# Kernel optimization log

Hardware: AMD Instinct MI355X
Metric: run time of the kernel (lower is better)

## Reference

```python
import jax, jax.numpy as jnp
import numpy as np

BITS = 8
BOUND = 2 ** (BITS - 1) - 1  # 127, symmetric int8 as in AQT IntNumerics


def setup_inputs() -> dict:
    key = jax.random.key(0)
    k1, k2 = jax.random.split(key)
    lhs = jax.random.normal(k1, (8192, 4096), dtype=jnp.float32)
    rhs = jax.random.normal(k2, (4096, 4096), dtype=jnp.float32)
    return {"lhs": lhs, "rhs": rhs}


def reference(lhs, rhs):
    # Per-channel symmetric scales over the contracting dim (AQT calibration:
    # abs-max / bound). lhs contracts axis 1, rhs contracts axis 0, per
    # dimension_numbers (((1,),(0,)),((),())).
    lhs_scale = jnp.max(jnp.abs(lhs), axis=1, keepdims=True) / BOUND  # [M,1]
    rhs_scale = jnp.max(jnp.abs(rhs), axis=0, keepdims=True) / BOUND  # [1,N]
    lhs_scale = jnp.where(lhs_scale == 0, jnp.ones_like(lhs_scale), lhs_scale)
    rhs_scale = jnp.where(rhs_scale == 0, jnp.ones_like(rhs_scale), rhs_scale)

    # Quantize: round-to-nearest, clip to [-127, 127], store as int8.
    qlhs = jnp.clip(jnp.round(lhs / lhs_scale), -BOUND, BOUND).astype(jnp.int8)
    qrhs = jnp.clip(jnp.round(rhs / rhs_scale), -BOUND, BOUND).astype(jnp.int8)

    # Integer matmul with int32 accumulation (the AQT quantized dot_general).
    acc = jax.lax.dot_general(
        qlhs, qrhs,
        dimension_numbers=(((1,), (0,)), ((), ())),
        preferred_element_type=jnp.int32,
    )  # [M, N] int32

    # Inline dequant by transposed scales (scale_t): [M,1] * [1,N].
    return acc.astype(jnp.float32) * lhs_scale * rhs_scale
```

## Files before the change

kernel.cpp:

```cpp
#include <hip/hip_runtime.h>
#include <stdint.h>

#define M_DIM 8192
#define N_DIM 4096
#define K_DIM 4096

typedef int v4i __attribute__((ext_vector_type(4)));

typedef __attribute__((address_space(1))) const void gas_void;
typedef __attribute__((address_space(3))) void las_void;

__device__ __forceinline__ void async_copy16(const uint8_t* g, uint8_t* l) {
    __builtin_amdgcn_global_load_lds((gas_void*)g, (las_void*)l, 16, 0, 0);
}

__device__ __forceinline__ int quant1(float x, float scale) {
    float q = __builtin_rintf(x / scale);
    q = fminf(127.0f, fmaxf(-127.0f, q));
    return (int)q;
}

__device__ __forceinline__ uint32_t pack4(int q0, int q1, int q2, int q3) {
    return (uint32_t)(q0 & 255) | ((uint32_t)(q1 & 255) << 8) |
           ((uint32_t)(q2 & 255) << 16) | ((uint32_t)(q3 & 255) << 24);
}

__global__ __launch_bounds__(256) void quant_lhs_kernel(
    const float* __restrict__ lhs, uint8_t* __restrict__ qlhs,
    float* __restrict__ lhs_scale) {
    const int row = blockIdx.x;
    const int tid = threadIdx.x;
    const float4* src = (const float4*)(lhs + (size_t)row * K_DIM);

    float4 v[4];
    float m = 0.0f;
#pragma unroll
    for (int i = 0; i < 4; ++i) {
        v[i] = src[tid + i * 256];
        m = fmaxf(m, fmaxf(fmaxf(fabsf(v[i].x), fabsf(v[i].y)),
                           fmaxf(fabsf(v[i].z), fabsf(v[i].w))));
    }
#pragma unroll
    for (int off = 32; off > 0; off >>= 1)
        m = fmaxf(m, __shfl_down(m, off, 64));

    __shared__ float wmax[4];
    if ((tid & 63) == 0) wmax[tid >> 6] = m;
    __syncthreads();
    const float mm = fmaxf(fmaxf(wmax[0], wmax[1]), fmaxf(wmax[2], wmax[3]));
    const float scale = (mm == 0.0f) ? 1.0f : mm / 127.0f;
    if (tid == 0) lhs_scale[row] = scale;

    uint32_t* dst = (uint32_t*)(qlhs + (size_t)row * K_DIM);
#pragma unroll
    for (int i = 0; i < 4; ++i) {
        dst[tid + i * 256] = pack4(quant1(v[i].x, scale), quant1(v[i].y, scale),
                                   quant1(v[i].z, scale), quant1(v[i].w, scale));
    }
}

__global__ __launch_bounds__(256) void rhs_max_kernel(
    const float* __restrict__ rhs, uint32_t* __restrict__ maxbits) {
    const int c4 = (blockIdx.x * 256 + threadIdx.x) * 4;
    const int r0 = blockIdx.y * 32;
    float m0 = 0.0f, m1 = 0.0f, m2 = 0.0f, m3 = 0.0f;
#pragma unroll
    for (int r = 0; r < 32; ++r) {
        const float4 v = *(const float4*)(rhs + (size_t)(r0 + r) * N_DIM + c4);
        m0 = fmaxf(m0, fabsf(v.x));
        m1 = fmaxf(m1, fabsf(v.y));
        m2 = fmaxf(m2, fabsf(v.z));
        m3 = fmaxf(m3, fabsf(v.w));
    }
    atomicMax(&maxbits[c4 + 0], __float_as_uint(m0));
    atomicMax(&maxbits[c4 + 1], __float_as_uint(m1));
    atomicMax(&maxbits[c4 + 2], __float_as_uint(m2));
    atomicMax(&maxbits[c4 + 3], __float_as_uint(m3));
}

__global__ __launch_bounds__(256) void quant_rhs_t_kernel(
    const float* __restrict__ rhs, const uint32_t* __restrict__ maxbits,
    uint8_t* __restrict__ qrhsT) {
    __shared__ __align__(16) uint8_t tile[64 * 132];
    const int nbase = blockIdx.x * 64;
    const int kbase = blockIdx.y * 128;
    const int tid = threadIdx.x;

    const int n0 = (tid & 15) * 4;
    float s[4];
#pragma unroll
    for (int j = 0; j < 4; ++j) {
        const float m = __uint_as_float(maxbits[nbase + n0 + j]);
        s[j] = (m == 0.0f) ? 1.0f : m / 127.0f;
    }

#pragma unroll
    for (int p = 0; p < 2; ++p) {
        const int k0 = (tid >> 4) * 4 + p * 64;
        int q[4][4];
#pragma unroll
        for (int i = 0; i < 4; ++i) {
            const float4 v = *(const float4*)(
                rhs + (size_t)(kbase + k0 + i) * N_DIM + nbase + n0);
            q[i][0] = quant1(v.x, s[0]);
            q[i][1] = quant1(v.y, s[1]);
            q[i][2] = quant1(v.z, s[2]);
            q[i][3] = quant1(v.w, s[3]);
        }
#pragma unroll
        for (int j = 0; j < 4; ++j) {
            *(uint32_t*)(tile + (n0 + j) * 132 + k0) =
                pack4(q[0][j], q[1][j], q[2][j], q[3][j]);
        }
    }
    __syncthreads();

#pragma unroll
    for (int p = 0; p < 2; ++p) {
        const int c = tid + p * 256;
        const int n = c >> 3;
        const int g = c & 7;
        uint32_t d[4];
#pragma unroll
        for (int w = 0; w < 4; ++w)
            d[w] = *(const uint32_t*)(tile + n * 132 + g * 16 + w * 4);
        uint4 u;
        u.x = d[0]; u.y = d[1]; u.z = d[2]; u.w = d[3];
        *(uint4*)(qrhsT + (size_t)(nbase + n) * K_DIM + kbase + g * 16) = u;
    }
}

__global__ __launch_bounds__(512, 2) void gemm_i8_kernel(
    const uint8_t* __restrict__ qlhs, const uint8_t* __restrict__ qrhsT,
    const float* __restrict__ lhs_scale, const uint32_t* __restrict__ maxbits,
    float* __restrict__ out) {
    extern __shared__ __align__(16) uint8_t smem[];

    const int tid = threadIdx.x;
    const int wave = tid >> 6;
    const int lane = tid & 63;

    const int obid = blockIdx.y * 16 + blockIdx.x;
    const int xcd = obid & 7;
    const int local = obid >> 3;
    const int ty = (xcd >> 1) * 8 + (local >> 3);
    const int tx = (xcd & 1) * 8 + (local & 7);
    const int bm = ty * 256;
    const int bn = tx * 256;

    const int srow = tid >> 2;
    const int gsrc = (((tid & 3) ^ ((tid >> 3) & 3)) << 4);
    const uint8_t* gA = qlhs + (size_t)(bm + srow) * K_DIM + gsrc;
    const uint8_t* gA2 = gA + (size_t)128 * K_DIM;
    const uint8_t* gB = qrhsT + (size_t)(bn + srow) * K_DIM + gsrc;
    const uint8_t* gB2 = gB + (size_t)128 * K_DIM;
    const uint32_t stO = (uint32_t)tid * 16u;

    const int wm = (wave >> 2) * 128;
    const int wn = (wave & 3) * 64;
    const uint32_t fg = (uint32_t)((((lane >> 4) ^ ((lane >> 1) & 3)) << 4));
    const uint32_t aoff = (uint32_t)((wm + (lane & 15)) * 64) + fg;
    const uint32_t boff = 16384u + (uint32_t)((wn + (lane & 15)) * 64) + fg;

    v4i acc[8][4] = {};

#define FENCE() asm volatile("" ::: "memory")
#define LGKM(n)                                                 \
    do {                                                        \
        asm volatile("s_waitcnt lgkmcnt(" #n ")" ::: "memory"); \
        __builtin_amdgcn_sched_barrier(0);                      \
    } while (0)
#define MFMA4(mi, av)                                                          \
    do {                                                                       \
        acc[mi][0] =                                                           \
            __builtin_amdgcn_mfma_i32_16x16x64_i8(av, vb0, acc[mi][0], 0, 0, 0); \
        acc[mi][1] =                                                           \
            __builtin_amdgcn_mfma_i32_16x16x64_i8(av, vb1, acc[mi][1], 0, 0, 0); \
        acc[mi][2] =                                                           \
            __builtin_amdgcn_mfma_i32_16x16x64_i8(av, vb2, acc[mi][2], 0, 0, 0); \
        acc[mi][3] =                                                           \
            __builtin_amdgcn_mfma_i32_16x16x64_i8(av, vb3, acc[mi][3], 0, 0, 0); \
    } while (0)

#pragma unroll
    for (int p = 0; p < 3; ++p) {
        uint8_t* sb = smem + (p << 15);
        async_copy16(gA, sb + stO);
        async_copy16(gA2, sb + 8192 + stO);
        async_copy16(gB, sb + 16384 + stO);
        async_copy16(gB2, sb + 24576 + stO);
        gA += 64; gA2 += 64; gB += 64; gB2 += 64;
    }
    asm volatile("s_waitcnt vmcnt(8)" ::: "memory");
    __builtin_amdgcn_s_barrier();

#pragma unroll 1
    for (int tt = 0; tt < 64; tt += 4) {
#pragma unroll
        for (int u = 0; u < 4; ++u) {
            const int t = tt + u;
            const uint8_t* const Cb = smem + (u << 15);
            uint8_t* const Sb = smem + (((u + 3) & 3) << 15);

            v4i vb0, vb1, vb2, vb3;
            v4i va0, va1, va2, va3, va4, va5, va6, va7;

            vb0 = *(const v4i*)(Cb + boff + 0);
            vb1 = *(const v4i*)(Cb + boff + 1024);
            vb2 = *(const v4i*)(Cb + boff + 2048);
            vb3 = *(const v4i*)(Cb + boff + 3072);
            va0 = *(const v4i*)(Cb + aoff + 0);
            FENCE();
            va1 = *(const v4i*)(Cb + aoff + 1024);
            FENCE();

            async_copy16(gA, Sb + stO);
            async_copy16(gA2, Sb + 8192 + stO);
            async_copy16(gB, Sb + 16384 + stO);
            async_copy16(gB2, Sb + 24576 + stO);
            if (t < 60) {
                gA += 64; gA2 += 64; gB += 64; gB2 += 64;
            }
            FENCE();

            __builtin_amdgcn_s_setprio(1);
            LGKM(1);  MFMA4(0, va0);
            va2 = *(const v4i*)(Cb + aoff + 2048); FENCE();
            LGKM(1);  MFMA4(1, va1);
            va3 = *(const v4i*)(Cb + aoff + 3072); FENCE();
            LGKM(1);  MFMA4(2, va2);
            va4 = *(const v4i*)(Cb + aoff + 4096); FENCE();
            LGKM(1);  MFMA4(3, va3);
            va5 = *(const v4i*)(Cb + aoff + 5120); FENCE();
            LGKM(1);  MFMA4(4, va4);
            va6 = *(const v4i*)(Cb + aoff + 6144); FENCE();
            LGKM(1);  MFMA4(5, va5);
            va7 = *(const v4i*)(Cb + aoff + 7168); FENCE();
            LGKM(1);  MFMA4(6, va6);
            LGKM(0);  MFMA4(7, va7);
            __builtin_amdgcn_s_setprio(0);

            asm volatile("s_waitcnt vmcnt(8)" ::: "memory");
            __builtin_amdgcn_s_barrier();
        }
    }
    asm volatile("s_waitcnt vmcnt(0)" ::: "memory");

    const int r0 = bm + wm + (lane >> 4) * 4;
    const int c0 = bn + wn + (lane & 15);
    float rsv[4];
#pragma unroll
    for (int ni = 0; ni < 4; ++ni) {
        const float m = __uint_as_float(maxbits[c0 + ni * 16]);
        rsv[ni] = (m == 0.0f) ? 1.0f : m / 127.0f;
    }
#pragma unroll
    for (int mi = 0; mi < 8; ++mi) {
        float ls[4];
#pragma unroll
        for (int r = 0; r < 4; ++r) ls[r] = lhs_scale[r0 + mi * 16 + r];
#pragma unroll
        for (int ni = 0; ni < 4; ++ni) {
            float* o = out + (size_t)(r0 + mi * 16) * N_DIM + c0 + ni * 16;
#pragma unroll
            for (int r = 0; r < 4; ++r)
                o[(size_t)r * N_DIM] = (float)acc[mi][ni][r] * ls[r] * rsv[ni];
        }
    }
#undef FENCE
#undef LGKM
#undef MFMA4
}

extern "C" void kernel_launch(void* const* d_in, const int* in_sizes, int n_in,
                              void* d_out, int out_size, void* d_ws,
                              size_t ws_size, hipStream_t stream) {
    const float* lhs = (const float*)d_in[0];
    const float* rhs = (const float*)d_in[1];
    float* out = (float*)d_out;

    uint8_t* ws = (uint8_t*)d_ws;
    uint8_t* qlhs = ws;
    uint8_t* qrhsT = ws + 33554432u;
    float* lhs_scale = (float*)(ws + 50331648u);
    uint32_t* maxbits = (uint32_t*)(ws + 50380800u);

    static bool attr_set = false;
    if (!attr_set) {
        hipFuncSetAttribute((const void*)gemm_i8_kernel,
                            hipFuncAttributeMaxDynamicSharedMemorySize,
                            131072);
        attr_set = true;
    }

    hipMemsetAsync(maxbits, 0, N_DIM * sizeof(uint32_t), stream);

    quant_lhs_kernel<<<M_DIM, 256, 0, stream>>>(lhs, qlhs, lhs_scale);
    rhs_max_kernel<<<dim3(N_DIM / 1024, 128), 256, 0, stream>>>(rhs, maxbits);
    quant_rhs_t_kernel<<<dim3(N_DIM / 64, K_DIM / 128), 256, 0, stream>>>(
        rhs, maxbits, qrhsT);
    gemm_i8_kernel<<<dim3(N_DIM / 256, M_DIM / 256), 512, 131072, stream>>>(
        qlhs, qrhsT, lhs_scale, maxbits, out);
}
```

Before: 408.9 us.

## Prefetch next tile's LDS fragments into ping-pong registers during MFMAs

Restructures the main loop so the B fragments and the first two A fragments of the next K-tile are read from LDS into an alternate register set (X/Y ping-pong) while the current tile's MFMAs run. The vmcnt wait tightens to 4, so after each barrier the next tile's data is resident and can be read early. This is meant to hide the LDS read latency at the start of each tile, which previously stalled the first MFMAs. The cost is higher VGPR pressure from the duplicated fragment registers and a hand-tuned lgkmcnt sequence that is easy to get wrong.

```diff
diff --git a/kernel.cpp b/kernel.cpp
--- a/kernel.cpp
+++ b/kernel.cpp
@@ -164,22 +164,79 @@
 
     v4i acc[8][4] = {};
 
+    v4i Xb0, Xb1, Xb2, Xb3, Xa0, Xa1;
+    v4i Yb0, Yb1, Yb2, Yb3, Ya0, Ya1;
+
 #define FENCE() asm volatile("" ::: "memory")
 #define LGKM(n)                                                 \
     do {                                                        \
         asm volatile("s_waitcnt lgkmcnt(" #n ")" ::: "memory"); \
         __builtin_amdgcn_sched_barrier(0);                      \
     } while (0)
-#define MFMA4(mi, av)                                                          \
+#define MFMA4(C, mi, av)                                                       \
     do {                                                                       \
-        acc[mi][0] =                                                           \
-            __builtin_amdgcn_mfma_i32_16x16x64_i8(av, vb0, acc[mi][0], 0, 0, 0); \
-        acc[mi][1] =                                                           \
-            __builtin_amdgcn_mfma_i32_16x16x64_i8(av, vb1, acc[mi][1], 0, 0, 0); \
-        acc[mi][2] =                                                           \
-            __builtin_amdgcn_mfma_i32_16x16x64_i8(av, vb2, acc[mi][2], 0, 0, 0); \
-        acc[mi][3] =                                                           \
-            __builtin_amdgcn_mfma_i32_16x16x64_i8(av, vb3, acc[mi][3], 0, 0, 0); \
+        acc[mi][0] = __builtin_amdgcn_mfma_i32_16x16x64_i8(av, C##b0,          \
+                                                           acc[mi][0], 0, 0, 0); \
+        acc[mi][1] = __builtin_amdgcn_mfma_i32_16x16x64_i8(av, C##b1,          \
+                                                           acc[mi][1], 0, 0, 0); \
+        acc[mi][2] = __builtin_amdgcn_mfma_i32_16x16x64_i8(av, C##b2,          \
+                                                           acc[mi][2], 0, 0, 0); \
+        acc[mi][3] = __builtin_amdgcn_mfma_i32_16x16x64_i8(av, C##b3,          \
+                                                           acc[mi][3], 0, 0, 0); \
+    } while (0)
+
+#define TILE(u, C, N)                                                   \
+    do {                                                                \
+        const uint8_t* const Cb = smem + ((u) << 15);                   \
+        const uint8_t* const Nb = smem + ((((u) + 1) & 3) << 15);       \
+        uint8_t* const Sb = smem + ((((u) + 3) & 3) << 15);             \
+               \
+        async_copy16(gA, Sb + stO);                                     \
+        async_copy16(gA2, Sb + 8192 + stO);                             \
+        async_copy16(gB, Sb + 16384 + stO);                             \
+        async_copy16(gB2, Sb + 24576 + stO);                            \
+        if (tt + (u) < 60) {                                            \
+            gA += 64; gA2 += 64; gB += 64; gB2 += 64;                   \
+        }                                                               \
+        FENCE();                                                        \
+        v4i va2, va3, va4, va5, va6, va7;                               \
+        va2 = *(const v4i*)(Cb + aoff + 2048);                          \
+        va3 = *(const v4i*)(Cb + aoff + 3072);                          \
+        FENCE();                                                        \
+        __builtin_amdgcn_s_setprio(1);                                  \
+        MFMA4(C, 0, C##a0);                                             \
+        va4 = *(const v4i*)(Cb + aoff + 4096);                          \
+        va5 = *(const v4i*)(Cb + aoff + 5120);                          \
+        FENCE();                                                        \
+        MFMA4(C, 1, C##a1);                                             \
+        va6 = *(const v4i*)(Cb + aoff + 6144);                          \
+        va7 = *(const v4i*)(Cb + aoff + 7168);                          \
+        FENCE();                                                        \
+        LGKM(5);                                                        \
+        MFMA4(C, 2, va2);                                               \
+        N##b0 = *(const v4i*)(Nb + boff + 0);                           \
+        N##b1 = *(const v4i*)(Nb + boff + 1024);                        \
+        N##b2 = *(const v4i*)(Nb + boff + 2048);                        \
+        N##b3 = *(const v4i*)(Nb + boff + 3072);                        \
+        FENCE();                                                        \
+        LGKM(8);                                                        \
+        MFMA4(C, 3, va3);                                               \
+        N##a0 = *(const v4i*)(Nb + aoff + 0);                           \
+        N##a1 = *(const v4i*)(Nb + aoff + 1024);                        \
+        FENCE();                                                        \
+        LGKM(9);                                                        \
+        MFMA4(C, 4, va4);                                               \
+        LGKM(8);                                                        \
+        MFMA4(C, 5, va5);                                               \
+        LGKM(7);                                                        \
+        MFMA4(C, 6, va6);                                               \
+        LGKM(6);                                                        \
+        MFMA4(C, 7, va7);                                               \
+        __builtin_amdgcn_s_setprio(0);                                  \
+        asm volatile("s_waitcnt vmcnt(4)" ::: "memory");                \
+        __builtin_amdgcn_s_barrier();                                   \
+        asm volatile("s_waitcnt lgkmcnt(0)" ::: "memory");              \
+        __builtin_amdgcn_sched_barrier(0);                              \
     } while (0)
 
 #pragma unroll
@@ -191,58 +248,24 @@
         async_copy16(gB2, sb + 24576 + stO);
         gA += 64; gA2 += 64; gB += 64; gB2 += 64;
     }
-    asm volatile("s_waitcnt vmcnt(8)" ::: "memory");
+    asm volatile("s_waitcnt vmcnt(4)" ::: "memory");
     __builtin_amdgcn_s_barrier();
+
+    Xb0 = *(const v4i*)(smem + boff + 0);
+    Xb1 = *(const v4i*)(smem + boff + 1024);
+    Xb2 = *(const v4i*)(smem + boff + 2048);
+    Xb3 = *(const v4i*)(smem + boff + 3072);
+    Xa0 = *(const v4i*)(smem + aoff + 0);
+    Xa1 = *(const v4i*)(smem + aoff + 1024);
+    asm volatile("s_waitcnt lgkmcnt(0)" ::: "memory");
+    __builtin_amdgcn_sched_barrier(0);
 
 #pragma unroll 1
     for (int tt = 0; tt < 64; tt += 4) {
-#pragma unroll
-        for (int u = 0; u < 4; ++u) {
-            const int t = tt + u;
-            const uint8_t* const Cb = smem + (u << 15);
-            uint8_t* const Sb = smem + (((u + 3) & 3) << 15);
-
-            v4i vb0, vb1, vb2, vb3;
-            v4i va0, va1, va2, va3, va4, va5, va6, va7;
-
-            vb0 = *(const v4i*)(Cb + boff + 0);
-            vb1 = *(const v4i*)(Cb + boff + 1024);
-            vb2 = *(const v4i*)(Cb + boff + 2048);
-            vb3 = *(const v4i*)(Cb + boff + 3072);
-            va0 = *(const v4i*)(Cb + aoff + 0);
-            FENCE();
-            va1 = *(const v4i*)(Cb + aoff + 1024);
-            FENCE();
-
-            async_copy16(gA, Sb + stO);
-            async_copy16(gA2, Sb + 8192 + stO);
-            async_copy16(gB, Sb + 16384 + stO);
-            async_copy16(gB2, Sb + 24576 + stO);
-            if (t < 60) {
-                gA += 64; gA2 += 64; gB += 64; gB2 += 64;
-            }
-            FENCE();
-
-            __builtin_amdgcn_s_setprio(1);
-            LGKM(1);  MFMA4(0, va0);
-            va2 = *(const v4i*)(Cb + aoff + 2048); FENCE();
-            LGKM(1);  MFMA4(1, va1);
-            va3 = *(const v4i*)(Cb + aoff + 3072); FENCE();
-            LGKM(1);  MFMA4(2, va2);
-            va4 = *(const v4i*)(Cb + aoff + 4096); FENCE();
-            LGKM(1);  MFMA4(3, va3);
-            va5 = *(const v4i*)(Cb + aoff + 5120); FENCE();
-            LGKM(1);  MFMA4(4, va4);
-            va6 = *(const v4i*)(Cb + aoff + 6144); FENCE();
-            LGKM(1);  MFMA4(5, va5);
-            va7 = *(const v4i*)(Cb + aoff + 7168); FENCE();
-            LGKM(1);  MFMA4(6, va6);
-            LGKM(0);  MFMA4(7, va7);
-            __builtin_amdgcn_s_setprio(0);
-
-            asm volatile("s_waitcnt vmcnt(8)" ::: "memory");
-            __builtin_amdgcn_s_barrier();
-        }
+        TILE(0, X, Y);
+        TILE(1, Y, X);
+        TILE(2, X, Y);
+        TILE(3, Y, X);
     }
     asm volatile("s_waitcnt vmcnt(0)" ::: "memory");
 
@@ -270,6 +293,7 @@
 #undef FENCE
 #undef LGKM
 #undef MFMA4
+#undef TILE
 }
 
 extern "C" void kernel_launch(void* const* d_in, const int* in_sizes, int n_in,
```

Measured after the change: 405.7 us. Within noise of the previous version (-0.8%).

## Load LHS MFMA fragments directly from global into registers, stage only RHS in LDS

Applied to the files above, without the earlier changes.

The int8 GEMM stops staging the A (lhs) tile through shared memory. Each wave now loads its A fragments straight from global memory into double-buffered registers, prefetched one k-step ahead, while only B goes through a 4-stage LDS ring that is half the previous size. This removes the A-side LDS traffic and the LDS reads on the MFMA critical path and halves the LDS footprint. The cost is more register pressure and uncoalesced 16-byte global loads for A, which waves sharing the same rows fetch redundantly, relying on L2/L1 to absorb it.

```diff
diff --git a/kernel.cpp b/kernel.cpp
--- a/kernel.cpp
+++ b/kernel.cpp
@@ -150,19 +150,24 @@
 
     const int srow = tid >> 2;
     const int gsrc = (((tid & 3) ^ ((tid >> 3) & 3)) << 4);
-    const uint8_t* gA = qlhs + (size_t)(bm + srow) * K_DIM + gsrc;
-    const uint8_t* gA2 = gA + (size_t)128 * K_DIM;
     const uint8_t* gB = qrhsT + (size_t)(bn + srow) * K_DIM + gsrc;
     const uint8_t* gB2 = gB + (size_t)128 * K_DIM;
     const uint32_t stO = (uint32_t)tid * 16u;
 
     const int wm = (wave >> 2) * 128;
     const int wn = (wave & 3) * 64;
+
     const uint32_t fg = (uint32_t)((((lane >> 4) ^ ((lane >> 1) & 3)) << 4));
-    const uint32_t aoff = (uint32_t)((wm + (lane & 15)) * 64) + fg;
-    const uint32_t boff = 16384u + (uint32_t)((wn + (lane & 15)) * 64) + fg;
+    const uint32_t boff = (uint32_t)((wn + (lane & 15)) * 64) + fg;
+
+    const uint8_t* gAf =
+        qlhs + (size_t)(bm + wm + (lane & 15)) * K_DIM + ((lane >> 4) * 16);
+#define AFS ((size_t)16 * K_DIM)
 
     v4i acc[8][4] = {};
+
+    v4i Xa0, Xa1, Xa2, Xa3, Xa4, Xa5, Xa6, Xa7;
+    v4i Ya0, Ya1, Ya2, Ya3, Ya4, Ya5, Ya6, Ya7;
 
 #define FENCE() asm volatile("" ::: "memory")
 #define LGKM(n)                                                 \
@@ -170,79 +175,93 @@
         asm volatile("s_waitcnt lgkmcnt(" #n ")" ::: "memory"); \
         __builtin_amdgcn_sched_barrier(0);                      \
     } while (0)
-#define MFMA4(mi, av)                                                          \
+#define VMW(n)                                                 \
+    do {                                                       \
+        asm volatile("s_waitcnt vmcnt(" #n ")" ::: "memory");  \
+        __builtin_amdgcn_sched_barrier(0);                     \
+    } while (0)
+#define MFMA8(C, ni, bv)                                                       \
     do {                                                                       \
-        acc[mi][0] =                                                           \
-            __builtin_amdgcn_mfma_i32_16x16x64_i8(av, vb0, acc[mi][0], 0, 0, 0); \
-        acc[mi][1] =                                                           \
-            __builtin_amdgcn_mfma_i32_16x16x64_i8(av, vb1, acc[mi][1], 0, 0, 0); \
-        acc[mi][2] =                                                           \
-            __builtin_amdgcn_mfma_i32_16x16x64_i8(av, vb2, acc[mi][2], 0, 0, 0); \
-        acc[mi][3] =                                                           \
-            __builtin_amdgcn_mfma_i32_16x16x64_i8(av, vb3, acc[mi][3], 0, 0, 0); \
+        acc[0][ni] = __builtin_amdgcn_mfma_i32_16x16x64_i8(C##a0, bv,          \
+                                                           acc[0][ni], 0, 0, 0); \
+        acc[1][ni] = __builtin_amdgcn_mfma_i32_16x16x64_i8(C##a1, bv,          \
+                                                           acc[1][ni], 0, 0, 0); \
+        acc[2][ni] = __builtin_amdgcn_mfma_i32_16x16x64_i8(C##a2, bv,          \
+                                                           acc[2][ni], 0, 0, 0); \
+        acc[3][ni] = __builtin_amdgcn_mfma_i32_16x16x64_i8(C##a3, bv,          \
+                                                           acc[3][ni], 0, 0, 0); \
+        acc[4][ni] = __builtin_amdgcn_mfma_i32_16x16x64_i8(C##a4, bv,          \
+                                                           acc[4][ni], 0, 0, 0); \
+        acc[5][ni] = __builtin_amdgcn_mfma_i32_16x16x64_i8(C##a5, bv,          \
+                                                           acc[5][ni], 0, 0, 0); \
+        acc[6][ni] = __builtin_amdgcn_mfma_i32_16x16x64_i8(C##a6, bv,          \
+                                                           acc[6][ni], 0, 0, 0); \
+        acc[7][ni] = __builtin_amdgcn_mfma_i32_16x16x64_i8(C##a7, bv,          \
+                                                           acc[7][ni], 0, 0, 0); \
     } while (0)
 
+#define TILE(u, CUR, NXT, t)                                            \
+    do {                                                                \
+        const uint8_t* const Cs = smem + ((u) << 14);                   \
+        uint8_t* const Ss = smem + ((((u) + 3) & 3) << 14);             \
+         \
+        NXT##a0 = *(const v4i*)(gAf + 0 * AFS);                         \
+        NXT##a1 = *(const v4i*)(gAf + 1 * AFS);                         \
+        NXT##a2 = *(const v4i*)(gAf + 2 * AFS);                         \
+        NXT##a3 = *(const v4i*)(gAf + 3 * AFS);                         \
+        NXT##a4 = *(const v4i*)(gAf + 4 * AFS);                         \
+        NXT##a5 = *(const v4i*)(gAf + 5 * AFS);                         \
+        NXT##a6 = *(const v4i*)(gAf + 6 * AFS);                         \
+        NXT##a7 = *(const v4i*)(gAf + 7 * AFS);                         \
+        FENCE();                                                        \
+                      \
+        async_copy16(gB, Ss + stO);                                     \
+        async_copy16(gB2, Ss + 8192 + stO);                             \
+        if ((t) < 60) { gB += 64; gB2 += 64; }                          \
+        if ((t) < 62) { gAf += 64; }                                    \
+        FENCE();                                                        \
+        v4i vb0 = *(const v4i*)(Cs + boff + 0);                         \
+        v4i vb1 = *(const v4i*)(Cs + boff + 1024);                      \
+        v4i vb2 = *(const v4i*)(Cs + boff + 2048);                      \
+        v4i vb3 = *(const v4i*)(Cs + boff + 3072);                      \
+        FENCE();                                                        \
+        __builtin_amdgcn_s_setprio(1);                                  \
+        LGKM(3); MFMA8(CUR, 0, vb0);                                    \
+        LGKM(2); MFMA8(CUR, 1, vb1);                                    \
+        LGKM(1); MFMA8(CUR, 2, vb2);                                    \
+        LGKM(0); MFMA8(CUR, 3, vb3);                                    \
+        __builtin_amdgcn_s_setprio(0);                                  \
+        VMW(2);             \
+        __builtin_amdgcn_s_barrier();                                   \
+    } while (0)
+
+    Xa0 = *(const v4i*)(gAf + 0 * AFS);
+    Xa1 = *(const v4i*)(gAf + 1 * AFS);
+    Xa2 = *(const v4i*)(gAf + 2 * AFS);
+    Xa3 = *(const v4i*)(gAf + 3 * AFS);
+    Xa4 = *(const v4i*)(gAf + 4 * AFS);
+    Xa5 = *(const v4i*)(gAf + 5 * AFS);
+    Xa6 = *(const v4i*)(gAf + 6 * AFS);
+    Xa7 = *(const v4i*)(gAf + 7 * AFS);
+    gAf += 64;
+    FENCE();
 #pragma unroll
     for (int p = 0; p < 3; ++p) {
-        uint8_t* sb = smem + (p << 15);
-        async_copy16(gA, sb + stO);
-        async_copy16(gA2, sb + 8192 + stO);
-        async_copy16(gB, sb + 16384 + stO);
-        async_copy16(gB2, sb + 24576 + stO);
-        gA += 64; gA2 += 64; gB += 64; gB2 += 64;
-    }
-    asm volatile("s_waitcnt vmcnt(8)" ::: "memory");
+        uint8_t* sb = smem + (p << 14);
+        async_copy16(gB, sb + stO);
+        async_copy16(gB2, sb + 8192 + stO);
+        gB += 64;
+        gB2 += 64;
+    }
+    VMW(4);
     __builtin_amdgcn_s_barrier();
 
 #pragma unroll 1
     for (int tt = 0; tt < 64; tt += 4) {
-#pragma unroll
-        for (int u = 0; u < 4; ++u) {
-            const int t = tt + u;
-            const uint8_t* const Cb = smem + (u << 15);
-            uint8_t* const Sb = smem + (((u + 3) & 3) << 15);
-
-            v4i vb0, vb1, vb2, vb3;
-            v4i va0, va1, va2, va3, va4, va5, va6, va7;
-
-            vb0 = *(const v4i*)(Cb + boff + 0);
-            vb1 = *(const v4i*)(Cb + boff + 1024);
-            vb2 = *(const v4i*)(Cb + boff + 2048);
-            vb3 = *(const v4i*)(Cb + boff + 3072);
-            va0 = *(const v4i*)(Cb + aoff + 0);
-            FENCE();
-            va1 = *(const v4i*)(Cb + aoff + 1024);
-            FENCE();
-
-            async_copy16(gA, Sb + stO);
-            async_copy16(gA2, Sb + 8192 + stO);
-            async_copy16(gB, Sb + 16384 + stO);
-            async_copy16(gB2, Sb + 24576 + stO);
-            if (t < 60) {
-                gA += 64; gA2 += 64; gB += 64; gB2 += 64;
-            }
-            FENCE();
-
-            __builtin_amdgcn_s_setprio(1);
-            LGKM(1);  MFMA4(0, va0);
-            va2 = *(const v4i*)(Cb + aoff + 2048); FENCE();
-            LGKM(1);  MFMA4(1, va1);
-            va3 = *(const v4i*)(Cb + aoff + 3072); FENCE();
-            LGKM(1);  MFMA4(2, va2);
-            va4 = *(const v4i*)(Cb + aoff + 4096); FENCE();
-            LGKM(1);  MFMA4(3, va3);
-            va5 = *(const v4i*)(Cb + aoff + 5120); FENCE();
-            LGKM(1);  MFMA4(4, va4);
-            va6 = *(const v4i*)(Cb + aoff + 6144); FENCE();
-            LGKM(1);  MFMA4(5, va5);
-            va7 = *(const v4i*)(Cb + aoff + 7168); FENCE();
-            LGKM(1);  MFMA4(6, va6);
-            LGKM(0);  MFMA4(7, va7);
-            __builtin_amdgcn_s_setprio(0);
-
-            asm volatile("s_waitcnt vmcnt(8)" ::: "memory");
-            __builtin_amdgcn_s_barrier();
-        }
+        TILE(0, X, Y, tt + 0);
+        TILE(1, Y, X, tt + 1);
+        TILE(2, X, Y, tt + 2);
+        TILE(3, Y, X, tt + 3);
     }
     asm volatile("s_waitcnt vmcnt(0)" ::: "memory");
 
@@ -269,7 +288,10 @@
     }
 #undef FENCE
 #undef LGKM
-#undef MFMA4
+#undef VMW
+#undef MFMA8
+#undef TILE
+#undef AFS
 }
 
 extern "C" void kernel_launch(void* const* d_in, const int* in_sizes, int n_in,
@@ -289,7 +311,7 @@
     if (!attr_set) {
         hipFuncSetAttribute((const void*)gemm_i8_kernel,
                             hipFuncAttributeMaxDynamicSharedMemorySize,
-                            131072);
+                            65536);
         attr_set = true;
     }
 
@@ -299,6 +321,6 @@
     rhs_max_kernel<<<dim3(N_DIM / 1024, 128), 256, 0, stream>>>(rhs, maxbits);
     quant_rhs_t_kernel<<<dim3(N_DIM / 64, K_DIM / 128), 256, 0, stream>>>(
         rhs, maxbits, qrhsT);
-    gemm_i8_kernel<<<dim3(N_DIM / 256, M_DIM / 256), 512, 131072, stream>>>(
+    gemm_i8_kernel<<<dim3(16, 32), 512, 65536, stream>>>(
         qlhs, qrhsT, lhs_scale, maxbits, out);
 }
```

Measured after the change: 582.8 us. 42.5% more time.
